# Kernel tuning notes

Hardware: AMD Instinct MI355X
Metric: run time of the kernel (lower is better)

Reference implementation:

```python
import jax, jax.numpy as jnp
import numpy as np

NUM_CLASSES = 20
NUM_ANCHORS = 5
INPUT_SIZE = 320.0
CONF_THR = 0.5
IOU_THR = 0.5
EPS = 1e-6
H = W = 40


def setup_inputs() -> dict:
    key = jax.random.key(0)
    x = jax.random.normal(key, (1, NUM_ANCHORS * (5 + NUM_CLASSES), H, W), dtype=jnp.float32)
    scaled_anchors = jnp.array(
        [[1.3221, 1.73145], [3.19275, 4.00944], [5.05587, 8.09892],
         [9.47112, 4.84053], [11.2364, 10.0071]], dtype=jnp.float32)
    return {"x": x, "scaled_anchors": scaled_anchors}


def decode(x, anchors):
    # x: (B, A*(5+C), H, W) -> boxes (B, A*H*W, 6) = [cx, cy, w, h, conf, cls]
    B, _, h, w = x.shape
    A = anchors.shape[0]
    stride_h = INPUT_SIZE / h
    stride_w = INPUT_SIZE / w
    pred = x.reshape(B, A, 5 + NUM_CLASSES, h, w).transpose(0, 1, 3, 4, 2)  # (B,A,H,W,5+C)
    tx = jax.nn.sigmoid(pred[..., 0])
    ty = jax.nn.sigmoid(pred[..., 1])
    tw = pred[..., 2]
    th = pred[..., 3]
    conf = jax.nn.sigmoid(pred[..., 4])
    cls_idx = jnp.argmax(jax.nn.sigmoid(pred[..., 5:]), axis=-1)  # (B,A,H,W)
    grid_x = jnp.arange(w, dtype=x.dtype)            # broadcasts along last axis
    grid_y = jnp.arange(h, dtype=x.dtype)[:, None]   # broadcasts along row axis
    aw = anchors[:, 0][None, :, None, None]
    ah = anchors[:, 1][None, :, None, None]
    bx = (tx + grid_x) * stride_w
    by = (ty + grid_y) * stride_h
    bw = jnp.exp(tw) * aw * stride_w
    bh = jnp.exp(th) * ah * stride_h
    boxes = jnp.stack([bx, by, bw, bh, conf], axis=-1).reshape(B, -1, 5)
    cls_f = cls_idx.reshape(B, -1, 1).astype(x.dtype)
    return jnp.concatenate([boxes, cls_f], axis=-1)


def nms(boxes6):
    # boxes6: (N, 6) [cx, cy, w, h, conf, cls]. Fixed-shape NMS: boxes are
    # sorted by conf desc; suppressed / low-conf boxes are zeroed out.
    order = jnp.argsort(-boxes6[:, 4])
    b = boxes6[order]
    valid = b[:, 4] > CONF_THR
    cx, cy, w, h, cls = b[:, 0], b[:, 1], b[:, 2], b[:, 3], b[:, 5]
    x1, y1 = cx - w / 2.0, cy - h / 2.0
    x2, y2 = cx + w / 2.0, cy + h / 2.0
    inter_w = jnp.clip(jnp.minimum(x2[:, None], x2[None, :]) - jnp.maximum(x1[:, None], x1[None, :]), 0)
    inter_h = jnp.clip(jnp.minimum(y2[:, None], y2[None, :]) - jnp.maximum(y1[:, None], y1[None, :]), 0)
    inter = inter_w * inter_h                       # (N, N)
    area = jnp.abs((x2 - x1) * (y2 - y1))
    iou = inter / (area[:, None] + area[None, :] - inter + EPS)
    N = b.shape[0]
    idx = jnp.arange(N)

    def body(i, keep):
        # kept box i suppresses later boxes of the same class with IoU >= thr
        sup = keep[i] & keep & (cls == cls[i]) & (iou[i] >= IOU_THR) & (idx > i)
        return keep & ~sup

    keep = jax.lax.fori_loop(0, N, body, valid)
    return b * keep[:, None].astype(b.dtype)


def reference(x, scaled_anchors):
    dec = decode(x, scaled_anchors)   # (1, N, 6)
    return nms(dec[0])                # (N, 6)
```

## Files before the change

### kernel.cpp

```cpp
#include <hip/hip_runtime.h>
#include <stdint.h>

#define NBOX 8000
#define NPAD 8192

#define COUNT_OFF 0
#define ECNT_OFF  4
#define VKEYS_OFF 0x9000
#define U_OFF     0x20000
#define UARR(i)   (U_OFF + (size_t)(i) * NPAD * 4)
#define SIDX_OFF  0x50000
#define SARR(i)   (0x58000 + (size_t)(i) * NPAD * 4)
#define EDGE_OFF  (size_t)0x200000

__device__ __forceinline__ float sigmoidf_(float x) {
    return 1.0f / (1.0f + expf(-x));
}

__global__ __launch_bounds__(64) void decode_kernel(const float* __restrict__ x,
                                                    const float* __restrict__ anchors,
                                                    unsigned char* __restrict__ ws) {
    int n = blockIdx.x * 64 + threadIdx.x;
    int a   = n / 1600;
    int pos = n - a * 1600;
    int gy  = pos / 40;
    int gx  = pos - gy * 40;
    const float* p = x + (size_t)a * 25 * 1600 + pos;

    float tx   = sigmoidf_(p[0]);
    float ty   = sigmoidf_(p[1600]);
    float tw   = p[2 * 1600];
    float th   = p[3 * 1600];
    float conf = sigmoidf_(p[4 * 1600]);

    float best = -1.0f; int bi = 0;
    #pragma unroll
    for (int c = 0; c < 20; ++c) {
        float v = sigmoidf_(p[(5 + c) * 1600]);
        if (v > best) { best = v; bi = c; }
    }

    float aw = anchors[a * 2 + 0];
    float ah = anchors[a * 2 + 1];
    float bx = (tx + (float)gx) * 8.0f;
    float by = (ty + (float)gy) * 8.0f;
    float bw = expf(tw) * aw * 8.0f;
    float bh = expf(th) * ah * 8.0f;

    ((float*)(ws + UARR(0)))[n] = bx;
    ((float*)(ws + UARR(1)))[n] = by;
    ((float*)(ws + UARR(2)))[n] = bw;
    ((float*)(ws + UARR(3)))[n] = bh;
    ((float*)(ws + UARR(4)))[n] = conf;
    ((float*)(ws + UARR(5)))[n] = (float)bi;

    bool valid = conf > 0.5f;
    unsigned long long bal = __ballot(valid);
    if (bal) {
        int lead = __builtin_ctzll(bal);
        unsigned int base = 0;
        if ((int)threadIdx.x == lead)
            base = atomicAdd((unsigned int*)(ws + COUNT_OFF), (unsigned int)__popcll(bal));
        base = (unsigned int)__shfl((int)base, lead, 64);
        if (valid) {
            unsigned int cb = __float_as_uint(conf);
            unsigned long long key = ((unsigned long long)cb << 32) | (unsigned long long)(8191 - n);
            unsigned int slot = base + (unsigned int)__popcll(bal & ((1ull << threadIdx.x) - 1ull));
            ((unsigned long long*)(ws + VKEYS_OFF))[slot] = key;
        }
    }
}

__global__ __launch_bounds__(256) void rank_scatter_kernel(unsigned char* __restrict__ ws) {
#pragma clang fp contract(off)
    __shared__ unsigned long long tile[256];
    __shared__ int partial[256];
    int V = *(const int*)(ws + COUNT_OFF);
    if (V > NPAD) V = NPAD;
    int tid  = threadIdx.x;
    int lane = tid & 63;
    int q    = tid >> 6;
    int b    = blockIdx.x;
    int i    = (b << 6) + lane;

    const unsigned long long* vk = (const unsigned long long*)(ws + VKEYS_OFF);
    unsigned long long ki = (i < V) ? vk[i] : ~0ull;
    int cnt = 0;
    if ((b << 6) < V) {
        int ntiles = (V + 255) >> 8;
        for (int tb = 0; tb < ntiles; ++tb) {
            int j = (tb << 8) + tid;
            tile[tid] = (j < V) ? vk[j] : 0ull;
            __syncthreads();
            int basej = (tb << 8) + (q << 6);
            int lim = V - basej;
            if (lim > 64) lim = 64;
            const unsigned long long* tq = &tile[q << 6];
            if (lim == 64) {
                #pragma unroll 16
                for (int jj = 0; jj < 64; ++jj) cnt += (tq[jj] > ki) ? 1 : 0;
            } else {
                for (int jj = 0; jj < lim; ++jj) cnt += (tq[jj] > ki) ? 1 : 0;
            }
            __syncthreads();
        }
    }
    partial[tid] = cnt;
    __syncthreads();
    if (q == 0) {
        float* sx1 = (float*)(ws + SARR(0));
        float* sy1 = (float*)(ws + SARR(1));
        float* sx2 = (float*)(ws + SARR(2));
        float* sy2 = (float*)(ws + SARR(3));
        float* sar = (float*)(ws + SARR(4));
        float* scl = (float*)(ws + SARR(5));
        if (i < V) {
            int r = partial[lane] + partial[64 + lane] + partial[128 + lane] + partial[192 + lane];
            int idx = 8191 - (int)(ki & 0x1FFFull);
            ((int*)(ws + SIDX_OFF))[r] = idx;
            float cx = ((float*)(ws + UARR(0)))[idx];
            float cy = ((float*)(ws + UARR(1)))[idx];
            float w  = ((float*)(ws + UARR(2)))[idx];
            float h  = ((float*)(ws + UARR(3)))[idx];
            float x1 = cx - w / 2.0f;
            float y1 = cy - h / 2.0f;
            float x2 = cx + w / 2.0f;
            float y2 = cy + h / 2.0f;
            sx1[r] = x1; sy1[r] = y1; sx2[r] = x2; sy2[r] = y2;
            sar[r] = fabsf((x2 - x1) * (y2 - y1));
            scl[r] = ((float*)(ws + UARR(5)))[idx];
        } else {
            ((int*)(ws + SIDX_OFF))[i] = -1;
            sx1[i] = 0.f; sy1[i] = 0.f; sx2[i] = 0.f; sy2[i] = 0.f;
            sar[i] = 0.f; scl[i] = -1.0f;
        }
    }
}

__global__ __launch_bounds__(256) void mask_kernel(unsigned char* __restrict__ ws) {
#pragma clang fp contract(off)
    int V = *(int*)(ws + COUNT_OFF);
    if (V > NPAD) V = NPAD;
    int i0 = blockIdx.y * 256;
    int w  = blockIdx.x;
    int j0 = w * 64;
    if (i0 >= V) return;
    if (j0 >= V) return;
    if (j0 + 64 <= i0) return;
    int tid  = threadIdx.x;
    int lane = tid & 63;
    int i    = i0 + tid;

    const float* sx1 = (const float*)(ws + SARR(0));
    const float* sy1 = (const float*)(ws + SARR(1));
    const float* sx2 = (const float*)(ws + SARR(2));
    const float* sy2 = (const float*)(ws + SARR(3));
    const float* sar = (const float*)(ws + SARR(4));
    const float* scl = (const float*)(ws + SARR(5));

    __shared__ float cx1[64], cy1[64], cx2[64], cy2[64], car[64], ccl[64];
    if (tid < 64) {
        int j = j0 + tid;
        cx1[tid] = sx1[j]; cy1[tid] = sy1[j];
        cx2[tid] = sx2[j]; cy2[tid] = sy2[j];
        car[tid] = sar[j]; ccl[tid] = scl[j];
    }
    __syncthreads();

    unsigned long long word = 0;
    if (i < V && j0 + 64 > i + 1) {
        float x1i = sx1[i], y1i = sy1[i], x2i = sx2[i], y2i = sy2[i];
        float ai = sar[i], ci = scl[i];
        for (int jj = 0; jj < 64; ++jj) {
            int j = j0 + jj;
            if (j <= i || j >= V) continue;
            if (ccl[jj] != ci) continue;
            float iw = fminf(x2i, cx2[jj]) - fmaxf(x1i, cx1[jj]);
            iw = fmaxf(iw, 0.0f);
            float ih = fminf(y2i, cy2[jj]) - fmaxf(y1i, cy1[jj]);
            ih = fmaxf(ih, 0.0f);
            float inter = iw * ih;
            float denom = ai + car[jj] - inter + 1e-6f;
            if (inter / denom >= 0.5f) word |= (1ull << jj);
        }
    }

    int pc = __popcll(word);
    int scan = pc;
    #pragma unroll
    for (int d = 1; d < 64; d <<= 1) {
        int t = __shfl_up(scan, d, 64);
        if (lane >= d) scan += t;
    }
    int total = __shfl(scan, 63, 64);
    unsigned int base = 0;
    if (total > 0) {
        if (lane == 63)
            base = atomicAdd((unsigned int*)(ws + ECNT_OFF), (unsigned int)total);
        base = (unsigned int)__shfl((int)base, 63, 64);
        unsigned int off = base + (unsigned int)(scan - pc);
        unsigned int* edges = (unsigned int*)(ws + EDGE_OFF);
        unsigned long long t = word;
        while (t) {
            int bit = __builtin_ctzll(t);
            t &= t - 1ull;
            edges[off++] = ((unsigned int)i << 13) | (unsigned int)(j0 + bit);
        }
    }
}

__global__ __launch_bounds__(1024, 1) void nms_out_kernel(unsigned char* __restrict__ ws,
                                                          float* __restrict__ out) {
    int tid = threadIdx.x;
    int V = *(const int*)(ws + COUNT_OFF);
    if (V > NPAD) V = NPAD;
    unsigned int E = *(const unsigned int*)(ws + ECNT_OFF);
    const unsigned int* edges = (const unsigned int*)(ws + EDGE_OFF);

    __shared__ unsigned long long alive[128], supp[128];
    __shared__ int flag;

    if (tid < 128) {
        int base = tid << 6;
        int rem = V - base;
        alive[tid] = (rem >= 64) ? ~0ull : (rem > 0 ? ((1ull << rem) - 1ull) : 0ull);
    }
    __syncthreads();

    for (;;) {
        if (tid < 128) supp[tid] = 0ull;
        __syncthreads();
        for (unsigned int e = tid; e < E; e += 1024) {
            unsigned int u = edges[e];
            unsigned int i = u >> 13, j = u & 8191u;
            if ((alive[i >> 6] >> (i & 63)) & 1ull)
                atomicOr(&supp[j >> 6], 1ull << (j & 63));
        }
        if (tid == 0) flag = 0;
        __syncthreads();
        if (tid < 128) {
            int base = tid << 6;
            int rem = V - base;
            unsigned long long init = (rem >= 64) ? ~0ull : (rem > 0 ? ((1ull << rem) - 1ull) : 0ull);
            unsigned long long na = init & ~supp[tid];
            if (na != alive[tid]) { alive[tid] = na; flag = 1; }
        }
        __syncthreads();
        if (!flag) break;
    }

    for (int r = tid; r < NBOX; r += 1024) {
        bool keep = (r < V) && ((alive[r >> 6] >> (r & 63)) & 1ull);
        float o0 = 0.f, o1 = 0.f, o2 = 0.f, o3 = 0.f, o4 = 0.f, o5 = 0.f;
        if (keep) {
            int idx = ((const int*)(ws + SIDX_OFF))[r];
            if (idx >= 0 && idx < NBOX) {
                o0 = ((const float*)(ws + UARR(0)))[idx];
                o1 = ((const float*)(ws + UARR(1)))[idx];
                o2 = ((const float*)(ws + UARR(2)))[idx];
                o3 = ((const float*)(ws + UARR(3)))[idx];
                o4 = ((const float*)(ws + UARR(4)))[idx];
                o5 = ((const float*)(ws + UARR(5)))[idx];
            }
        }
        out[r * 6 + 0] = o0;
        out[r * 6 + 1] = o1;
        out[r * 6 + 2] = o2;
        out[r * 6 + 3] = o3;
        out[r * 6 + 4] = o4;
        out[r * 6 + 5] = o5;
    }
}

extern "C" void kernel_launch(void* const* d_in, const int* in_sizes, int n_in,
                              void* d_out, int out_size, void* d_ws, size_t ws_size,
                              hipStream_t stream) {
    const float* x       = (const float*)d_in[0];
    const float* anchors = (const float*)d_in[1];
    float* out           = (float*)d_out;
    unsigned char* ws    = (unsigned char*)d_ws;

    hipMemsetAsync(ws, 0, 8, stream);
    decode_kernel<<<125, 64, 0, stream>>>(x, anchors, ws);
    rank_scatter_kernel<<<NPAD / 64, 256, 0, stream>>>(ws);
    dim3 mgrid(128, NPAD / 256);
    mask_kernel<<<mgrid, 256, 0, stream>>>(ws);
    nms_out_kernel<<<1, 1024, 0, stream>>>(ws, out);
}
```

Baseline: 131.6 us.

## Fuse decode and rank sort into one kernel, ranking all boxes by confidence

Merges the decode kernel and the rank/scatter kernel into a single kernel that recomputes confidence keys straight from the input and ranks all 8192 slots instead of only the valid ones. Each box is decoded and written directly to its sorted position, which removes the memset, one launch, the atomic compaction and the gather indirection. In exchange the rank loop always covers the full set, so it does more comparisons than before when few boxes pass the threshold. Validity is now derived from the sorted confidence array in the mask and final kernels.

Result: slower. 136.7 us (+3.9%).

```diff
diff --git a/kernel.cpp b/kernel.cpp
--- a/kernel.cpp
+++ b/kernel.cpp
@@ -4,176 +4,135 @@
 #define NBOX 8000
 #define NPAD 8192
 
-#define COUNT_OFF 0
-#define ECNT_OFF  4
-#define VKEYS_OFF 0x9000
-#define U_OFF     0x20000
-#define UARR(i)   (U_OFF + (size_t)(i) * NPAD * 4)
-#define SIDX_OFF  0x50000
-#define SARR(i)   (0x58000 + (size_t)(i) * NPAD * 4)
-#define EDGE_OFF  (size_t)0x200000
+#define ECNT_OFF 0
+#define SB(i)    (0x10000 + (size_t)(i) * 0x8000)
+#define EDGE_OFF (size_t)0x200000
 
 __device__ __forceinline__ float sigmoidf_(float x) {
     return 1.0f / (1.0f + expf(-x));
 }
 
-__global__ __launch_bounds__(64) void decode_kernel(const float* __restrict__ x,
-                                                    const float* __restrict__ anchors,
-                                                    unsigned char* __restrict__ ws) {
-    int n = blockIdx.x * 64 + threadIdx.x;
-    int a   = n / 1600;
-    int pos = n - a * 1600;
-    int gy  = pos / 40;
-    int gx  = pos - gy * 40;
-    const float* p = x + (size_t)a * 25 * 1600 + pos;
-
-    float tx   = sigmoidf_(p[0]);
-    float ty   = sigmoidf_(p[1600]);
-    float tw   = p[2 * 1600];
-    float th   = p[3 * 1600];
-    float conf = sigmoidf_(p[4 * 1600]);
-
-    float best = -1.0f; int bi = 0;
-    #pragma unroll
-    for (int c = 0; c < 20; ++c) {
-        float v = sigmoidf_(p[(5 + c) * 1600]);
-        if (v > best) { best = v; bi = c; }
-    }
-
-    float aw = anchors[a * 2 + 0];
-    float ah = anchors[a * 2 + 1];
-    float bx = (tx + (float)gx) * 8.0f;
-    float by = (ty + (float)gy) * 8.0f;
-    float bw = expf(tw) * aw * 8.0f;
-    float bh = expf(th) * ah * 8.0f;
-
-    ((float*)(ws + UARR(0)))[n] = bx;
-    ((float*)(ws + UARR(1)))[n] = by;
-    ((float*)(ws + UARR(2)))[n] = bw;
-    ((float*)(ws + UARR(3)))[n] = bh;
-    ((float*)(ws + UARR(4)))[n] = conf;
-    ((float*)(ws + UARR(5)))[n] = (float)bi;
-
-    bool valid = conf > 0.5f;
-    unsigned long long bal = __ballot(valid);
-    if (bal) {
-        int lead = __builtin_ctzll(bal);
-        unsigned int base = 0;
-        if ((int)threadIdx.x == lead)
-            base = atomicAdd((unsigned int*)(ws + COUNT_OFF), (unsigned int)__popcll(bal));
-        base = (unsigned int)__shfl((int)base, lead, 64);
-        if (valid) {
-            unsigned int cb = __float_as_uint(conf);
-            unsigned long long key = ((unsigned long long)cb << 32) | (unsigned long long)(8191 - n);
-            unsigned int slot = base + (unsigned int)__popcll(bal & ((1ull << threadIdx.x) - 1ull));
-            ((unsigned long long*)(ws + VKEYS_OFF))[slot] = key;
-        }
-    }
-}
-
-__global__ __launch_bounds__(256) void rank_scatter_kernel(unsigned char* __restrict__ ws) {
-#pragma clang fp contract(off)
+__global__ __launch_bounds__(256) void sort_decode_kernel(const float* __restrict__ x,
+                                                          const float* __restrict__ anchors,
+                                                          unsigned char* __restrict__ ws) {
     __shared__ unsigned long long tile[256];
     __shared__ int partial[256];
-    int V = *(const int*)(ws + COUNT_OFF);
-    if (V > NPAD) V = NPAD;
     int tid  = threadIdx.x;
     int lane = tid & 63;
     int q    = tid >> 6;
     int b    = blockIdx.x;
     int i    = (b << 6) + lane;
 
-    const unsigned long long* vk = (const unsigned long long*)(ws + VKEYS_OFF);
-    unsigned long long ki = (i < V) ? vk[i] : ~0ull;
+    if (b == 0 && tid == 0) *(unsigned int*)(ws + ECNT_OFF) = 0u;
+
+    unsigned long long ki;
+    if (i < NBOX) {
+        int a = i / 1600, pos = i - a * 1600;
+        float c = sigmoidf_(x[a * 40000 + 4 * 1600 + pos]);
+        ki = ((unsigned long long)__float_as_uint(c) << 32) | (unsigned long long)(8191 - i);
+    } else {
+        ki = (unsigned long long)(8191 - i);
+    }
+
     int cnt = 0;
-    if ((b << 6) < V) {
-        int ntiles = (V + 255) >> 8;
-        for (int tb = 0; tb < ntiles; ++tb) {
-            int j = (tb << 8) + tid;
-            tile[tid] = (j < V) ? vk[j] : 0ull;
-            __syncthreads();
-            int basej = (tb << 8) + (q << 6);
-            int lim = V - basej;
-            if (lim > 64) lim = 64;
-            const unsigned long long* tq = &tile[q << 6];
-            if (lim == 64) {
-                #pragma unroll 16
-                for (int jj = 0; jj < 64; ++jj) cnt += (tq[jj] > ki) ? 1 : 0;
-            } else {
-                for (int jj = 0; jj < lim; ++jj) cnt += (tq[jj] > ki) ? 1 : 0;
+    for (int tb = 0; tb < 32; ++tb) {
+        int j = (tb << 8) + tid;
+        unsigned long long kj;
+        if (j < NBOX) {
+            int aj = j / 1600, posj = j - aj * 1600;
+            float cj = sigmoidf_(x[aj * 40000 + 4 * 1600 + posj]);
+            kj = ((unsigned long long)__float_as_uint(cj) << 32) | (unsigned long long)(8191 - j);
+        } else {
+            kj = (unsigned long long)(8191 - j);
+        }
+        tile[tid] = kj;
+        __syncthreads();
+        const unsigned long long* tq = &tile[q << 6];
+        #pragma unroll 16
+        for (int jj = 0; jj < 64; ++jj) cnt += (tq[jj] > ki) ? 1 : 0;
+        __syncthreads();
+    }
+    partial[tid] = cnt;
+    __syncthreads();
+
+    if (q == 0) {
+        int r = partial[lane] + partial[64 + lane] + partial[128 + lane] + partial[192 + lane];
+        float bx = 0.f, by = 0.f, bw = 0.f, bh = 0.f, conf = 0.f, cls = -1.0f;
+        if (i < NBOX) {
+            int a = i / 1600, pos = i - a * 1600;
+            int gy = pos / 40, gx = pos - gy * 40;
+            const float* p = x + (size_t)a * 40000 + pos;
+            float tx = sigmoidf_(p[0]);
+            float ty = sigmoidf_(p[1600]);
+            float tw = p[2 * 1600];
+            float th = p[3 * 1600];
+            conf = sigmoidf_(p[4 * 1600]);
+            float best = -1.0f; int bi = 0;
+            #pragma unroll
+            for (int c = 0; c < 20; ++c) {
+                float v = sigmoidf_(p[(5 + c) * 1600]);
+                if (v > best) { best = v; bi = c; }
             }
-            __syncthreads();
-        }
-    }
-    partial[tid] = cnt;
-    __syncthreads();
-    if (q == 0) {
-        float* sx1 = (float*)(ws + SARR(0));
-        float* sy1 = (float*)(ws + SARR(1));
-        float* sx2 = (float*)(ws + SARR(2));
-        float* sy2 = (float*)(ws + SARR(3));
-        float* sar = (float*)(ws + SARR(4));
-        float* scl = (float*)(ws + SARR(5));
-        if (i < V) {
-            int r = partial[lane] + partial[64 + lane] + partial[128 + lane] + partial[192 + lane];
-            int idx = 8191 - (int)(ki & 0x1FFFull);
-            ((int*)(ws + SIDX_OFF))[r] = idx;
-            float cx = ((float*)(ws + UARR(0)))[idx];
-            float cy = ((float*)(ws + UARR(1)))[idx];
-            float w  = ((float*)(ws + UARR(2)))[idx];
-            float h  = ((float*)(ws + UARR(3)))[idx];
-            float x1 = cx - w / 2.0f;
-            float y1 = cy - h / 2.0f;
-            float x2 = cx + w / 2.0f;
-            float y2 = cy + h / 2.0f;
-            sx1[r] = x1; sy1[r] = y1; sx2[r] = x2; sy2[r] = y2;
-            sar[r] = fabsf((x2 - x1) * (y2 - y1));
-            scl[r] = ((float*)(ws + UARR(5)))[idx];
-        } else {
-            ((int*)(ws + SIDX_OFF))[i] = -1;
-            sx1[i] = 0.f; sy1[i] = 0.f; sx2[i] = 0.f; sy2[i] = 0.f;
-            sar[i] = 0.f; scl[i] = -1.0f;
+            float aw = anchors[a * 2 + 0];
+            float ah = anchors[a * 2 + 1];
+            bx = (tx + (float)gx) * 8.0f;
+            by = (ty + (float)gy) * 8.0f;
+            bw = expf(tw) * aw * 8.0f;
+            bh = expf(th) * ah * 8.0f;
+            cls = (float)bi;
+        }
+        {
+        #pragma clang fp contract(off)
+            float x1 = bx - bw / 2.0f, y1 = by - bh / 2.0f;
+            float x2 = bx + bw / 2.0f, y2 = by + bh / 2.0f;
+            float ar = fabsf((x2 - x1) * (y2 - y1));
+            ((float*)(ws + SB(0)))[r]  = bx;  ((float*)(ws + SB(1)))[r]  = by;
+            ((float*)(ws + SB(2)))[r]  = bw;  ((float*)(ws + SB(3)))[r]  = bh;
+            ((float*)(ws + SB(4)))[r]  = conf; ((float*)(ws + SB(5)))[r] = cls;
+            ((float*)(ws + SB(6)))[r]  = x1;  ((float*)(ws + SB(7)))[r]  = y1;
+            ((float*)(ws + SB(8)))[r]  = x2;  ((float*)(ws + SB(9)))[r]  = y2;
+            ((float*)(ws + SB(10)))[r] = ar;
         }
     }
 }
 
 __global__ __launch_bounds__(256) void mask_kernel(unsigned char* __restrict__ ws) {
 #pragma clang fp contract(off)
-    int V = *(int*)(ws + COUNT_OFF);
-    if (V > NPAD) V = NPAD;
+    const float* sconf = (const float*)(ws + SB(4));
     int i0 = blockIdx.y * 256;
     int w  = blockIdx.x;
     int j0 = w * 64;
-    if (i0 >= V) return;
-    if (j0 >= V) return;
+    if (sconf[i0] <= 0.5f) return;
+    if (sconf[j0] <= 0.5f) return;
     if (j0 + 64 <= i0) return;
     int tid  = threadIdx.x;
     int lane = tid & 63;
     int i    = i0 + tid;
 
-    const float* sx1 = (const float*)(ws + SARR(0));
-    const float* sy1 = (const float*)(ws + SARR(1));
-    const float* sx2 = (const float*)(ws + SARR(2));
-    const float* sy2 = (const float*)(ws + SARR(3));
-    const float* sar = (const float*)(ws + SARR(4));
-    const float* scl = (const float*)(ws + SARR(5));
-
-    __shared__ float cx1[64], cy1[64], cx2[64], cy2[64], car[64], ccl[64];
+    const float* sx1 = (const float*)(ws + SB(6));
+    const float* sy1 = (const float*)(ws + SB(7));
+    const float* sx2 = (const float*)(ws + SB(8));
+    const float* sy2 = (const float*)(ws + SB(9));
+    const float* sar = (const float*)(ws + SB(10));
+    const float* scl = (const float*)(ws + SB(5));
+
+    __shared__ float cx1[64], cy1[64], cx2[64], cy2[64], car[64], ccl[64], ccf[64];
     if (tid < 64) {
         int j = j0 + tid;
         cx1[tid] = sx1[j]; cy1[tid] = sy1[j];
         cx2[tid] = sx2[j]; cy2[tid] = sy2[j];
-        car[tid] = sar[j]; ccl[tid] = scl[j];
+        car[tid] = sar[j]; ccl[tid] = scl[j]; ccf[tid] = sconf[j];
     }
     __syncthreads();
 
     unsigned long long word = 0;
-    if (i < V && j0 + 64 > i + 1) {
+    if (sconf[i] > 0.5f && j0 + 64 > i + 1) {
         float x1i = sx1[i], y1i = sy1[i], x2i = sx2[i], y2i = sy2[i];
         float ai = sar[i], ci = scl[i];
         for (int jj = 0; jj < 64; ++jj) {
             int j = j0 + jj;
-            if (j <= i || j >= V) continue;
+            if (j <= i) continue;
+            if (ccf[jj] <= 0.5f) continue;
             if (ccl[jj] != ci) continue;
             float iw = fminf(x2i, cx2[jj]) - fmaxf(x1i, cx1[jj]);
             iw = fmaxf(iw, 0.0f);
@@ -193,8 +152,8 @@
         if (lane >= d) scan += t;
     }
     int total = __shfl(scan, 63, 64);
-    unsigned int base = 0;
     if (total > 0) {
+        unsigned int base = 0;
         if (lane == 63)
             base = atomicAdd((unsigned int*)(ws + ECNT_OFF), (unsigned int)total);
         base = (unsigned int)__shfl((int)base, 63, 64);
@@ -211,20 +170,21 @@
 
 __global__ __launch_bounds__(1024, 1) void nms_out_kernel(unsigned char* __restrict__ ws,
                                                           float* __restrict__ out) {
-    int tid = threadIdx.x;
-    int V = *(const int*)(ws + COUNT_OFF);
-    if (V > NPAD) V = NPAD;
+    int tid  = threadIdx.x;
+    int lane = tid & 63;
     unsigned int E = *(const unsigned int*)(ws + ECNT_OFF);
     const unsigned int* edges = (const unsigned int*)(ws + EDGE_OFF);
-
-    __shared__ unsigned long long alive[128], supp[128];
+    const float* sconf = (const float*)(ws + SB(4));
+
+    __shared__ unsigned long long valid[128], alive[128], supp[128];
     __shared__ int flag;
 
-    if (tid < 128) {
-        int base = tid << 6;
-        int rem = V - base;
-        alive[tid] = (rem >= 64) ? ~0ull : (rem > 0 ? ((1ull << rem) - 1ull) : 0ull);
-    }
+    for (int c = tid >> 6; c < 128; c += 16) {
+        unsigned long long m = __ballot(sconf[(c << 6) + lane] > 0.5f);
+        if (lane == 0) valid[c] = m;
+    }
+    __syncthreads();
+    if (tid < 128) alive[tid] = valid[tid];
     __syncthreads();
 
     for (;;) {
@@ -239,10 +199,7 @@
         if (tid == 0) flag = 0;
         __syncthreads();
         if (tid < 128) {
-            int base = tid << 6;
-            int rem = V - base;
-            unsigned long long init = (rem >= 64) ? ~0ull : (rem > 0 ? ((1ull << rem) - 1ull) : 0ull);
-            unsigned long long na = init & ~supp[tid];
+            unsigned long long na = valid[tid] & ~supp[tid];
             if (na != alive[tid]) { alive[tid] = na; flag = 1; }
         }
         __syncthreads();
@@ -250,18 +207,15 @@
     }
 
     for (int r = tid; r < NBOX; r += 1024) {
-        bool keep = (r < V) && ((alive[r >> 6] >> (r & 63)) & 1ull);
+        bool keep = (alive[r >> 6] >> (r & 63)) & 1ull;
         float o0 = 0.f, o1 = 0.f, o2 = 0.f, o3 = 0.f, o4 = 0.f, o5 = 0.f;
         if (keep) {
-            int idx = ((const int*)(ws + SIDX_OFF))[r];
-            if (idx >= 0 && idx < NBOX) {
-                o0 = ((const float*)(ws + UARR(0)))[idx];
-                o1 = ((const float*)(ws + UARR(1)))[idx];
-                o2 = ((const float*)(ws + UARR(2)))[idx];
-                o3 = ((const float*)(ws + UARR(3)))[idx];
-                o4 = ((const float*)(ws + UARR(4)))[idx];
-                o5 = ((const float*)(ws + UARR(5)))[idx];
-            }
+            o0 = ((const float*)(ws + SB(0)))[r];
+            o1 = ((const float*)(ws + SB(1)))[r];
+            o2 = ((const float*)(ws + SB(2)))[r];
+            o3 = ((const float*)(ws + SB(3)))[r];
+            o4 = ((const float*)(ws + SB(4)))[r];
+            o5 = ((const float*)(ws + SB(5)))[r];
         }
         out[r * 6 + 0] = o0;
         out[r * 6 + 1] = o1;
@@ -280,9 +234,7 @@
     float* out           = (float*)d_out;
     unsigned char* ws    = (unsigned char*)d_ws;
 
-    hipMemsetAsync(ws, 0, 8, stream);
-    decode_kernel<<<125, 64, 0, stream>>>(x, anchors, ws);
-    rank_scatter_kernel<<<NPAD / 64, 256, 0, stream>>>(ws);
+    sort_decode_kernel<<<NPAD / 64, 256, 0, stream>>>(x, anchors, ws);
     dim3 mgrid(128, NPAD / 256);
     mask_kernel<<<mgrid, 256, 0, stream>>>(ws);
     nms_out_kernel<<<1, 1024, 0, stream>>>(ws, out);
```
